# Performance work log

Measured on AMD Instinct MI355X. Metric: run time of the kernel, lower is better.

The kernel has to match this reference:

```python
import jax, jax.numpy as jnp
import numpy as np

NH = 4
ATT = 16
COL = 64
AIS = 64
B = 8192
SK = 200


def setup_inputs() -> dict:
    key = jax.random.key(0)
    k1, k2, k3, k4, k5 = jax.random.split(key, 5)
    # Xavier-uniform bounds for [fan_in, fan_out] matrices
    def xavier(k, fan_in, fan_out):
        bound = float(np.sqrt(6.0 / (fan_in + fan_out)))
        return jax.random.uniform(k, (fan_in, fan_out), jnp.float32, -bound, bound)
    return {
        "query_input": jax.random.normal(k1, (B, 1, COL), jnp.float32),
        "action_list_input": jax.random.normal(k2, (B, SK, AIS), jnp.float32),
        "Q": xavier(k3, COL, ATT * NH),
        "K": xavier(k4, AIS, ATT * NH),
        "V": xavier(k5, AIS, ATT * NH),
    }


def reference(query_input, action_list_input, Q, K, V):
    b = query_input.shape[0]
    sq = query_input.shape[1]          # == 1 (required by final reshape)
    sk = action_list_input.shape[1]
    # projections
    q = jnp.tensordot(query_input, Q, axes=([-1], [0]))        # [B,Sq,NH*ATT]
    k = jnp.tensordot(action_list_input, K, axes=([-1], [0]))  # [B,Sk,NH*ATT]
    v = jnp.tensordot(action_list_input, V, axes=([-1], [0]))  # [B,Sk,NH*ATT]
    # split heads: chunk along last dim then stack on new leading dim -> [NH,B,S,ATT]
    qh = jnp.transpose(q.reshape(b, sq, NH, ATT), (2, 0, 1, 3))
    kh = jnp.transpose(k.reshape(b, sk, NH, ATT), (2, 0, 1, 3))
    vh = jnp.transpose(v.reshape(b, sk, NH, ATT), (2, 0, 1, 3))
    scores = jnp.einsum("hbqd,hbkd->hbqk", qh, kh) / 8.0       # [NH,B,Sq,Sk]
    attn = jax.nn.softmax(scores, axis=-1)
    res = jnp.einsum("hbqk,hbkd->hbqd", attn, vh)              # [NH,B,Sq,ATT]
    res = jnp.transpose(res, (1, 2, 0, 3))                     # [B,Sq,NH,ATT]
    return res.reshape(b, NH * ATT)
```

## Files before the change

kernel.cpp:

```cpp
#include <hip/hip_runtime.h>

#define NH   4
#define ATT  16
#define COL  64
#define AIS  64
#define SK   200
#define HD   64
#define JP   32
#define AROW 33

typedef _Float16 half2v __attribute__((ext_vector_type(2)));
typedef unsigned int uint32;

static __device__ __forceinline__ half2v u2h(uint32 u) {
    union { uint32 u; half2v h; } x; x.u = u; return x.h;
}

static __device__ __forceinline__ uint32 pk_u32(float a, float b) {
#if __has_builtin(__builtin_amdgcn_cvt_pkrtz)
    union { decltype(__builtin_amdgcn_cvt_pkrtz(0.f, 0.f)) h; uint32 u; } x;
    x.h = __builtin_amdgcn_cvt_pkrtz(a, b);
    return x.u;
#else
    union { half2v h; uint32 u; } x;
    x.h.x = (_Float16)a; x.h.y = (_Float16)b;
    return x.u;
#endif
}

#if __has_builtin(__builtin_amdgcn_fdot2)
#define DOT2(a, b, c) __builtin_amdgcn_fdot2((a), (b), (c), false)
#else
#define DOT2(a, b, c) fmaf((float)(a).x, (float)(b).x, fmaf((float)(a).y, (float)(b).y, (c)))
#endif

__global__ __launch_bounds__(256)
void qk_kernel(const float* __restrict__ query, const float* __restrict__ Qw,
               const float* __restrict__ Kw, uint32* __restrict__ qk2, int nb) {
    __shared__ float qh_s[HD];
    const int t = threadIdx.x;
    #pragma unroll
    for (int bb = 0; bb < 4; ++bb) {
        const int b = blockIdx.x * 4 + bb;
        if (b >= nb) break;
        const float* qb = query + (size_t)b * COL;
        if (t < HD) {
            float acc = 0.f;
            #pragma unroll
            for (int c = 0; c < COL; ++c)
                acc = fmaf(qb[c], Qw[c * HD + t], acc);
            qh_s[t] = acc;
        }
        __syncthreads();
        if (t < 128) {
            const int h = t >> 5, jp = t & 31;
            float a0 = 0.f, a1 = 0.f;
            #pragma unroll
            for (int d = 0; d < ATT; ++d) {
                const float q = qh_s[h * ATT + d];
                a0 = fmaf(q, Kw[(2 * jp)     * HD + h * ATT + d], a0);
                a1 = fmaf(q, Kw[(2 * jp + 1) * HD + h * ATT + d], a1);
            }
            qk2[(size_t)b * 128 + t] = pk_u32(a0 * 0.125f, a1 * 0.125f);
        }
        __syncthreads();
    }
}

__global__ __launch_bounds__(256, 4)
void attn_kernel(const float* __restrict__ action, const float* __restrict__ Vw,
                 const uint32* __restrict__ qk2, float* __restrict__ out) {
    __shared__ uint32 A2[SK * AROW];
    __shared__ float4 p4_s[SK];
    __shared__ float4 wpart[4][64];
    __shared__ float4 w4_s[64];
    __shared__ float  invd_s[NH];

    const int b    = blockIdx.x;
    const int t    = threadIdx.x;
    const int lane = t & 63;
    const int wv   = t >> 6;

    const float4* act4 = (const float4*)(action + (size_t)b * (SK * AIS));
    #pragma unroll
    for (int i = 0; i < 13; ++i) {
        const int idx = i * 256 + t;
        if (idx < SK * AIS / 4) {
            const float4 v = act4[idx];
            const int k   = idx >> 4;
            const int jp0 = (idx & 15) * 2;
            A2[k * AROW + jp0]     = pk_u32(v.x, v.y);
            A2[k * AROW + jp0 + 1] = pk_u32(v.z, v.w);
        }
    }
    __syncthreads();

    const uint32* qkb = qk2 + (size_t)b * 128;
    if (t < SK) {
        float a0 = 0.f, a1 = 0.f, a2 = 0.f, a3 = 0.f;
        const int base = t * AROW;
        #pragma unroll 8
        for (int jp = 0; jp < JP; ++jp) {
            const half2v av = u2h(A2[base + jp]);
            a0 = DOT2(av, u2h(qkb[jp]),      a0);
            a1 = DOT2(av, u2h(qkb[32 + jp]), a1);
            a2 = DOT2(av, u2h(qkb[64 + jp]), a2);
            a3 = DOT2(av, u2h(qkb[96 + jp]), a3);
        }
        float4 s; s.x = a0; s.y = a1; s.z = a2; s.w = a3;
        p4_s[t] = s;
    }
    __syncthreads();

    {
        float* pf = (float*)p4_s;
        const int h = wv;
        const float s0 = pf[lane * 4 + h];
        const float s1 = pf[(lane + 64) * 4 + h];
        const float s2 = pf[(lane + 128) * 4 + h];
        const float s3 = (lane < SK - 192) ? pf[(lane + 192) * 4 + h] : -1e30f;
        float m = fmaxf(fmaxf(s0, s1), fmaxf(s2, s3));
        #pragma unroll
        for (int off = 32; off; off >>= 1) m = fmaxf(m, __shfl_xor(m, off));
        const float e0 = __expf(s0 - m);
        const float e1 = __expf(s1 - m);
        const float e2 = __expf(s2 - m);
        const float e3 = (lane < SK - 192) ? __expf(s3 - m) : 0.f;
        pf[lane * 4 + h]         = e0;
        pf[(lane + 64) * 4 + h]  = e1;
        pf[(lane + 128) * 4 + h] = e2;
        if (lane < SK - 192) pf[(lane + 192) * 4 + h] = e3;
        float sum = e0 + e1 + e2 + e3;
        #pragma unroll
        for (int off = 32; off; off >>= 1) sum += __shfl_xor(sum, off);
        if (lane == 0) invd_s[h] = 1.f / sum;
    }
    __syncthreads();

    {
        const int j  = lane;
        const int jp = j >> 1;
        const int k0 = wv * 50;
        float c0 = 0.f, c1 = 0.f, c2 = 0.f, c3 = 0.f;
        #pragma unroll 10
        for (int kk = 0; kk < 50; ++kk) {
            const int k = k0 + kk;
            const float4 p = p4_s[k];
            const half2v av = u2h(A2[k * AROW + jp]);
            const float a = (j & 1) ? (float)av.y : (float)av.x;
            c0 = fmaf(p.x, a, c0);
            c1 = fmaf(p.y, a, c1);
            c2 = fmaf(p.z, a, c2);
            c3 = fmaf(p.w, a, c3);
        }
        float4 c; c.x = c0; c.y = c1; c.z = c2; c.w = c3;
        wpart[wv][j] = c;
    }
    __syncthreads();

    if (t < 64) {
        const float4 r0 = wpart[0][t], r1 = wpart[1][t];
        const float4 r2 = wpart[2][t], r3 = wpart[3][t];
        float4 w;
        w.x = (r0.x + r1.x + r2.x + r3.x) * invd_s[0];
        w.y = (r0.y + r1.y + r2.y + r3.y) * invd_s[1];
        w.z = (r0.z + r1.z + r2.z + r3.z) * invd_s[2];
        w.w = (r0.w + r1.w + r2.w + r3.w) * invd_s[3];
        w4_s[t] = w;
    }
    __syncthreads();

    if (t < 64) {
        const int h = t >> 4;
        const float* wf = (const float*)w4_s;
        float acc = 0.f;
        #pragma unroll
        for (int j = 0; j < AIS; ++j)
            acc = fmaf(wf[j * 4 + h], Vw[j * HD + t], acc);
        out[(size_t)b * HD + t] = acc;
    }
}

extern "C" void kernel_launch(void* const* d_in, const int* in_sizes, int n_in,
                              void* d_out, int out_size, void* d_ws, size_t ws_size,
                              hipStream_t stream) {
    const float* query  = (const float*)d_in[0];
    const float* action = (const float*)d_in[1];
    const float* Qw     = (const float*)d_in[2];
    const float* Kw     = (const float*)d_in[3];
    const float* Vw     = (const float*)d_in[4];
    float* outp = (float*)d_out;

    const int B = in_sizes[0] / COL;
    uint32* qk2 = (uint32*)d_ws;

    qk_kernel<<<(B + 3) / 4, 256, 0, stream>>>(query, Qw, Kw, qk2, B);
    attn_kernel<<<B, 256, 0, stream>>>(action, Vw, qk2, outp);
}
```

Baseline: 578.4 us.

## Fuse query-key projection into attention kernel and prefetch action tile into registers

```diff
diff --git a/kernel.cpp b/kernel.cpp
--- a/kernel.cpp
+++ b/kernel.cpp
@@ -34,47 +34,20 @@
 #define DOT2(a, b, c) fmaf((float)(a).x, (float)(b).x, fmaf((float)(a).y, (float)(b).y, (c)))
 #endif
 
-__global__ __launch_bounds__(256)
-void qk_kernel(const float* __restrict__ query, const float* __restrict__ Qw,
-               const float* __restrict__ Kw, uint32* __restrict__ qk2, int nb) {
-    __shared__ float qh_s[HD];
-    const int t = threadIdx.x;
-    #pragma unroll
-    for (int bb = 0; bb < 4; ++bb) {
-        const int b = blockIdx.x * 4 + bb;
-        if (b >= nb) break;
-        const float* qb = query + (size_t)b * COL;
-        if (t < HD) {
-            float acc = 0.f;
-            #pragma unroll
-            for (int c = 0; c < COL; ++c)
-                acc = fmaf(qb[c], Qw[c * HD + t], acc);
-            qh_s[t] = acc;
-        }
-        __syncthreads();
-        if (t < 128) {
-            const int h = t >> 5, jp = t & 31;
-            float a0 = 0.f, a1 = 0.f;
-            #pragma unroll
-            for (int d = 0; d < ATT; ++d) {
-                const float q = qh_s[h * ATT + d];
-                a0 = fmaf(q, Kw[(2 * jp)     * HD + h * ATT + d], a0);
-                a1 = fmaf(q, Kw[(2 * jp + 1) * HD + h * ATT + d], a1);
-            }
-            qk2[(size_t)b * 128 + t] = pk_u32(a0 * 0.125f, a1 * 0.125f);
-        }
-        __syncthreads();
-    }
-}
-
 __global__ __launch_bounds__(256, 4)
-void attn_kernel(const float* __restrict__ action, const float* __restrict__ Vw,
-                 const uint32* __restrict__ qk2, float* __restrict__ out) {
+void fused_attn_kernel(const float* __restrict__ query,
+                       const float* __restrict__ action,
+                       const float* __restrict__ Qw,
+                       const float* __restrict__ Kw,
+                       const float* __restrict__ Vw,
+                       float* __restrict__ out) {
     __shared__ uint32 A2[SK * AROW];
     __shared__ float4 p4_s[SK];
     __shared__ float4 wpart[4][64];
     __shared__ float4 w4_s[64];
     __shared__ float  invd_s[NH];
+    __shared__ float  qh_s[HD];
+    __shared__ __align__(16) uint32 qk4_s[JP * 4];
 
     const int b    = blockIdx.x;
     const int t    = threadIdx.x;
@@ -82,30 +55,64 @@
     const int wv   = t >> 6;
 
     const float4* act4 = (const float4*)(action + (size_t)b * (SK * AIS));
+    float4 sv[13];
     #pragma unroll
-    for (int i = 0; i < 13; ++i) {
+    for (int i = 0; i < 12; ++i) sv[i] = act4[i * 256 + t];
+    if (t < 128) sv[12] = act4[3072 + t];
+
+    const float* qb = query + (size_t)b * COL;
+    if (t < HD) {
+        float acc = 0.f;
+        #pragma unroll
+        for (int c = 0; c < COL; ++c)
+            acc = fmaf(qb[c], Qw[c * HD + t], acc);
+        qh_s[t] = acc;
+    }
+    __syncthreads();
+
+    if (t < 128) {
+        const int h = t >> 5, jp = t & 31;
+        float a0 = 0.f, a1 = 0.f;
+        #pragma unroll
+        for (int d = 0; d < ATT; ++d) {
+            const float q = qh_s[h * ATT + d];
+            a0 = fmaf(q, Kw[(2 * jp)     * HD + h * ATT + d], a0);
+            a1 = fmaf(q, Kw[(2 * jp + 1) * HD + h * ATT + d], a1);
+        }
+        qk4_s[jp * 4 + h] = pk_u32(a0 * 0.125f, a1 * 0.125f);
+    }
+
+    #pragma unroll
+    for (int i = 0; i < 12; ++i) {
         const int idx = i * 256 + t;
-        if (idx < SK * AIS / 4) {
-            const float4 v = act4[idx];
-            const int k   = idx >> 4;
-            const int jp0 = (idx & 15) * 2;
-            A2[k * AROW + jp0]     = pk_u32(v.x, v.y);
-            A2[k * AROW + jp0 + 1] = pk_u32(v.z, v.w);
-        }
-    }
-    __syncthreads();
-
-    const uint32* qkb = qk2 + (size_t)b * 128;
+        const float4 v = sv[i];
+        const int k   = idx >> 4;
+        const int jp0 = (idx & 15) * 2;
+        A2[k * AROW + jp0]     = pk_u32(v.x, v.y);
+        A2[k * AROW + jp0 + 1] = pk_u32(v.z, v.w);
+    }
+    if (t < 128) {
+        const int idx = 3072 + t;
+        const float4 v = sv[12];
+        const int k   = idx >> 4;
+        const int jp0 = (idx & 15) * 2;
+        A2[k * AROW + jp0]     = pk_u32(v.x, v.y);
+        A2[k * AROW + jp0 + 1] = pk_u32(v.z, v.w);
+    }
+    __syncthreads();
+
     if (t < SK) {
         float a0 = 0.f, a1 = 0.f, a2 = 0.f, a3 = 0.f;
         const int base = t * AROW;
+        const uint4* qk4 = (const uint4*)qk4_s;
         #pragma unroll 8
         for (int jp = 0; jp < JP; ++jp) {
             const half2v av = u2h(A2[base + jp]);
-            a0 = DOT2(av, u2h(qkb[jp]),      a0);
-            a1 = DOT2(av, u2h(qkb[32 + jp]), a1);
-            a2 = DOT2(av, u2h(qkb[64 + jp]), a2);
-            a3 = DOT2(av, u2h(qkb[96 + jp]), a3);
+            const uint4 q4 = qk4[jp];
+            a0 = DOT2(av, u2h(q4.x), a0);
+            a1 = DOT2(av, u2h(q4.y), a1);
+            a2 = DOT2(av, u2h(q4.z), a2);
+            a3 = DOT2(av, u2h(q4.w), a3);
         }
         float4 s; s.x = a0; s.y = a1; s.z = a2; s.w = a3;
         p4_s[t] = s;
@@ -191,9 +198,8 @@
     const float* Vw     = (const float*)d_in[4];
     float* outp = (float*)d_out;
 
+    (void)d_ws; (void)ws_size;
+
     const int B = in_sizes[0] / COL;
-    uint32* qk2 = (uint32*)d_ws;
-
-    qk_kernel<<<(B + 3) / 4, 256, 0, stream>>>(query, Qw, Kw, qk2, B);
-    attn_kernel<<<B, 256, 0, stream>>>(action, Vw, qk2, outp);
-}
+    fused_attn_kernel<<<B, 256, 0, stream>>>(query, action, Qw, Kw, Vw, outp);
+}
```

After: 545.3 us. 5.7% less time.
